# Performance work log

Measured on AMD Instinct MI355X. Metric: run time of the kernel, lower is better.

The kernel has to match this reference:

```python
import jax, jax.numpy as jnp
import numpy as np

EPS = float(np.finfo(np.float32).eps)
BN_EPS = 1e-5
TOP_K = 3


def _dist_squared(p1, p2):
    # p1: [B,N,3], p2: [B,S,3] -> [B,N,S]
    d = -2.0 * jnp.einsum('bnc,bsc->bns', p1, p2)
    d = d + jnp.sum(p1 * p1, axis=-1, keepdims=True)
    d = d + jnp.sum(p2 * p2, axis=-1)[:, None, :]
    return d


def _bn_gelu(x, gamma, beta):
    # training-mode BatchNorm1d over (batch, points), then exact GELU
    m = jnp.mean(x, axis=(0, 1))
    v = jnp.var(x, axis=(0, 1))
    xn = (x - m) * jax.lax.rsqrt(v + BN_EPS)
    return jax.nn.gelu(xn * gamma + beta, approximate=False)


def setup_inputs() -> dict:
    key = jax.random.key(0)
    ks = jax.random.split(key, 8)
    B, S, N, F, C = 8, 2048, 8192, 256, 128
    d_in, d_h, d_out = C + F, 512, 512
    return {
        'super_xyz': jax.random.normal(ks[0], (B, S, 3), jnp.float32),
        'super_point_features': jax.random.normal(ks[1], (B, S, F), jnp.float32),
        'xyz': jax.random.normal(ks[2], (B, N, 3), jnp.float32),
        'point_features': jax.random.normal(ks[3], (B, N, C), jnp.float32),
        'W1': jax.random.normal(ks[4], (d_in, d_h), jnp.float32) * 0.02,
        'g1': jnp.ones((d_h,), jnp.float32),
        'b1': jnp.zeros((d_h,), jnp.float32),
        'W2': jax.random.normal(ks[5], (d_h, d_out), jnp.float32) * 0.02,
        'g2': jnp.ones((d_out,), jnp.float32),
        'b2': jnp.zeros((d_out,), jnp.float32),
    }


def reference(super_xyz, super_point_features, xyz, point_features,
              W1, g1, b1, W2, g2, b2):
    d2 = _dist_squared(xyz, super_xyz)                 # [B,N,S]
    neg_vals, idx = jax.lax.top_k(-d2, TOP_K)          # smallest-k
    dists = jnp.maximum(-neg_vals, 0.0)                # [B,N,K]
    w = 1.0 / (dists + EPS)
    w = w / jnp.sum(w, axis=2, keepdims=True)
    gathered = jax.vmap(lambda f, i: f[i])(super_point_features, idx)  # [B,N,K,F]
    interp = jnp.sum(gathered * w[..., None], axis=2)  # [B,N,F]
    x = jnp.concatenate([point_features, interp], axis=-1)
    x = _bn_gelu(x @ W1, g1, b1)
    x = _bn_gelu(x @ W2, g2, b2)
    return x
```

## Files before the change

kernel.cpp:

```cpp
#include <hip/hip_runtime.h>
#include <hip/hip_bf16.h>


#define MROWS 65536
#define SPTS  2048
#define NPTS  8192
#define NCHUNK 8
#define CHUNK  (SPTS / NCHUNK)
#define EPSF  1.1920928955078125e-07f

typedef __bf16 v8bf __attribute__((ext_vector_type(8)));
typedef float  v4f  __attribute__((ext_vector_type(4)));

__device__ __forceinline__ float bf2f(unsigned short u) {
    union { unsigned u; float f; } v; v.u = ((unsigned)u) << 16; return v.f;
}
__device__ __forceinline__ unsigned short f2bf(float f) {
    union { float f; unsigned u; } v; v.f = f;
    unsigned r = v.u + 0x7fffu + ((v.u >> 16) & 1u);
    return (unsigned short)(r >> 16);
}
__device__ __forceinline__ float2 bf2x(unsigned u) {
    union { unsigned q; float f; } lo, hi;
    lo.q = u << 16; hi.q = u & 0xffff0000u;
    return make_float2(lo.f, hi.f);
}
__device__ __forceinline__ float ldf(const void* p, size_t i, bool bf) {
    return bf ? bf2f(((const unsigned short*)p)[i]) : ((const float*)p)[i];
}
__device__ __forceinline__ bool is_bf16_flag(const unsigned* dt) {
    return *dt == 0x3F803F80u;
}
__device__ __forceinline__ void gld16(const unsigned short* g, unsigned short* l) {
    __builtin_amdgcn_global_load_lds((const __attribute__((address_space(1))) void*)g,
                                     (__attribute__((address_space(3))) void*)l, 16, 0, 0);
}
__device__ __forceinline__ unsigned wmix(unsigned a, unsigned b, unsigned c,
                                         float w0, float w1, float w2) {
    float2 fa = bf2x(a), fb = bf2x(b), fc = bf2x(c);
    float lo = w0 * fa.x + w1 * fb.x + w2 * fc.x;
    float hi = w0 * fa.y + w1 * fb.y + w2 * fc.y;
    return ((unsigned)f2bf(hi) << 16) | (unsigned)f2bf(lo);
}
__device__ __forceinline__ uint2 pack4(float4 v) {
    uint2 r;
    r.x = ((unsigned)f2bf(v.y) << 16) | (unsigned)f2bf(v.x);
    r.y = ((unsigned)f2bf(v.w) << 16) | (unsigned)f2bf(v.z);
    return r;
}

__global__ __launch_bounds__(256) void transpose_w(const void* __restrict__ W,
                                                   unsigned short* __restrict__ WT,
                                                   int K, int N, const unsigned* dt) {
    bool bf = is_bf16_flag(dt);
    int idx = blockIdx.x * 256 + threadIdx.x;
    if (idx >= K * N) return;
    int n = idx / K, k = idx - n * K;
    WT[idx] = f2bf(ldf(W, (size_t)k * N + n, bf));
}

__global__ __launch_bounds__(256) void knn_scan(const void* __restrict__ sxyz_g,
                                                const void* __restrict__ xyz_g,
                                                double* __restrict__ pd,
                                                int* __restrict__ pi,
                                                const unsigned* dt) {
    const bool bf = is_bf16_flag(dt);
    __shared__ double sx[CHUNK], sy[CHUNK], sz[CHUNK], sn[CHUNK];
    const int b = blockIdx.y, c = blockIdx.z, tid = threadIdx.x;

    {
        int s = c * CHUNK + tid;
        size_t off = ((size_t)b * SPTS + s) * 3;
        float x, y, z;
        if (bf) {
            const unsigned short* p = (const unsigned short*)sxyz_g + off;
            x = bf2f(p[0]); y = bf2f(p[1]); z = bf2f(p[2]);
        } else {
            const float* p = (const float*)sxyz_g + off;
            x = p[0]; y = p[1]; z = p[2];
        }
        double dx = (double)x, dy = (double)y, dz = (double)z;
        sx[tid] = dx; sy[tid] = dy; sz[tid] = dz;
        sn[tid] = dx * dx + dy * dy + dz * dz;
    }
    __syncthreads();

    const int n = blockIdx.x * 256 + tid;
    size_t poff = ((size_t)b * NPTS + n) * 3;
    float px, py, pz;
    if (bf) {
        const unsigned short* p = (const unsigned short*)xyz_g + poff;
        px = bf2f(p[0]); py = bf2f(p[1]); pz = bf2f(p[2]);
    } else {
        const float* p = (const float*)xyz_g + poff;
        px = p[0]; py = p[1]; pz = p[2];
    }
    const double pxd = (double)px, pyd = (double)py, pzd = (double)pz;
    const double n1 = pxd * pxd + pyd * pyd + pzd * pzd;

    double d0 = 1e300, d1 = 1e300, d2 = 1e300;
    int i0 = 0, i1 = 0, i2 = 0;
    #pragma unroll 4
    for (int s = 0; s < CHUNK; ++s) {
        double dot = pxd * sx[s] + pyd * sy[s] + pzd * sz[s];
        double d = -2.0 * dot + n1 + sn[s];
        if (d < d2) {
            int gi = c * CHUNK + s;
            if (d < d1) {
                d2 = d1; i2 = i1;
                if (d < d0) { d1 = d0; i1 = i0; d0 = d; i0 = gi; }
                else        { d1 = d;  i1 = gi; }
            } else { d2 = d; i2 = gi; }
        }
    }
    size_t base = ((size_t)c * MROWS + (size_t)b * NPTS + n) * 3;
    pd[base] = d0; pd[base + 1] = d1; pd[base + 2] = d2;
    pi[base] = i0; pi[base + 1] = i1; pi[base + 2] = i2;
}

__global__ __launch_bounds__(256) void knn_weights(const double* __restrict__ pd,
                                                   const int* __restrict__ pi,
                                                   char* __restrict__ wi) {
    const int g = blockIdx.x * 256 + threadIdx.x;

    double d0 = 1e300, d1 = 1e300, d2 = 1e300;
    int i0 = 0, i1 = 0, i2 = 0;
    #pragma unroll
    for (int c = 0; c < NCHUNK; ++c) {
        size_t base = ((size_t)c * MROWS + g) * 3;
        #pragma unroll
        for (int j = 0; j < 3; ++j) {
            double d = pd[base + j];
            int gi = pi[base + j];
            if (d < d2) {
                if (d < d1) {
                    d2 = d1; i2 = i1;
                    if (d < d0) { d1 = d0; i1 = i0; d0 = d; i0 = gi; }
                    else        { d1 = d;  i1 = gi; }
                } else { d2 = d; i2 = gi; }
            }
        }
    }
    d0 = d0 > 0.0 ? d0 : 0.0;
    d1 = d1 > 0.0 ? d1 : 0.0;
    d2 = d2 > 0.0 ? d2 : 0.0;
    const double ED = (double)EPSF;
    double w0d = 1.0 / (d0 + ED), w1d = 1.0 / (d1 + ED), w2d = 1.0 / (d2 + ED);
    double wsd = w0d + w1d + w2d;
    float w0 = (float)(w0d / wsd), w1 = (float)(w1d / wsd), w2 = (float)(w2d / wsd);

    uint4 iv; iv.x = (unsigned)i0; iv.y = (unsigned)i1; iv.z = (unsigned)i2; iv.w = 0u;
    float4 wv = make_float4(w0, w1, w2, 0.0f);
    *(uint4*)(wi + (size_t)g * 32) = iv;
    *(float4*)(wi + (size_t)g * 32 + 16) = wv;
}

__global__ __launch_bounds__(256) void knn_interp(const char* __restrict__ wi,
                                                  const void* __restrict__ spf_g,
                                                  const void* __restrict__ pf_g,
                                                  unsigned short* __restrict__ x0,
                                                  const unsigned* dt) {
    const bool bf = is_bf16_flag(dt);
    const int tid = threadIdx.x;
    const int pl  = tid >> 4;
    const int sub = tid & 15;
    const int g   = blockIdx.x * 16 + pl;
    const int b   = g >> 13;

    const uint4  iv = *(const uint4*)(wi + (size_t)g * 32);
    const float4 wv = *(const float4*)(wi + (size_t)g * 32 + 16);
    const int i0 = (int)iv.x, i1 = (int)iv.y, i2 = (int)iv.z;
    const float w0 = wv.x, w1 = wv.y, w2 = wv.z;

    unsigned short* xr = x0 + (size_t)g * 384;
    uint4* xo = (uint4*)xr;

    if (bf) {
        const uint4* pp = (const uint4*)((const unsigned short*)pf_g + (size_t)g * 128);
        xo[sub] = pp[sub];
        const unsigned short* sb = (const unsigned short*)spf_g + (size_t)b * SPTS * 256;
        const uint4* fa = (const uint4*)(sb + (size_t)i0 * 256);
        const uint4* fb = (const uint4*)(sb + (size_t)i1 * 256);
        const uint4* fc = (const uint4*)(sb + (size_t)i2 * 256);
        #pragma unroll
        for (int r = 0; r < 2; ++r) {
            int j = sub + 16 * r;
            uint4 ua = fa[j], ub = fb[j], uc = fc[j], o;
            o.x = wmix(ua.x, ub.x, uc.x, w0, w1, w2);
            o.y = wmix(ua.y, ub.y, uc.y, w0, w1, w2);
            o.z = wmix(ua.z, ub.z, uc.z, w0, w1, w2);
            o.w = wmix(ua.w, ub.w, uc.w, w0, w1, w2);
            xo[16 + j] = o;
        }
    } else {
        const float4* pp = (const float4*)((const float*)pf_g + (size_t)g * 128);
        float4 v0 = pp[2 * sub], v1 = pp[2 * sub + 1];
        uint2 pa = pack4(v0), pb = pack4(v1);
        uint4 w; w.x = pa.x; w.y = pa.y; w.z = pb.x; w.w = pb.y;
        xo[sub] = w;
        const float* sb = (const float*)spf_g + (size_t)b * SPTS * 256;
        const float4* fa = (const float4*)(sb + (size_t)i0 * 256);
        const float4* fb = (const float4*)(sb + (size_t)i1 * 256);
        const float4* fc = (const float4*)(sb + (size_t)i2 * 256);
        #pragma unroll
        for (int r = 0; r < 2; ++r) {
            int j = sub + 16 * r;
            float4 a0 = fa[2 * j], a1 = fa[2 * j + 1];
            float4 b0 = fb[2 * j], b1 = fb[2 * j + 1];
            float4 c0 = fc[2 * j], c1 = fc[2 * j + 1];
            float4 r0, r1;
            r0.x = w0 * a0.x + w1 * b0.x + w2 * c0.x;
            r0.y = w0 * a0.y + w1 * b0.y + w2 * c0.y;
            r0.z = w0 * a0.z + w1 * b0.z + w2 * c0.z;
            r0.w = w0 * a0.w + w1 * b0.w + w2 * c0.w;
            r1.x = w0 * a1.x + w1 * b1.x + w2 * c1.x;
            r1.y = w0 * a1.y + w1 * b1.y + w2 * c1.y;
            r1.z = w0 * a1.z + w1 * b1.z + w2 * c1.z;
            r1.w = w0 * a1.w + w1 * b1.w + w2 * c1.w;
            uint2 q0 = pack4(r0), q1 = pack4(r1);
            uint4 o; o.x = q0.x; o.y = q0.y; o.z = q1.x; o.w = q1.y;
            xo[16 + j] = o;
        }
    }
}

template<bool CF32>
__global__ __launch_bounds__(256) void gemm_bt(const unsigned short* __restrict__ A,
                                               const unsigned short* __restrict__ BT,
                                               void* __restrict__ C,
                                               int M, int N, int K) {
    __shared__ unsigned short As[128 * 32];
    __shared__ unsigned short Bs[128 * 32];
    const int tid = threadIdx.x;
    const int m0 = blockIdx.x * 128, n0 = blockIdx.y * 128;
    const int lane = tid & 63, wave = tid >> 6;
    const int wm = (wave >> 1) * 64, wn = (wave & 1) * 64;
    const int l15 = lane & 15, quad = lane >> 4;

    const int o0 = tid * 16, o1 = o0 + 4096;
    const int ar0 = o0 >> 6, ac0 = (o0 & 63) >> 1;
    const int ar1 = o1 >> 6, ac1 = (o1 & 63) >> 1;
    const unsigned short* a0 = A + (size_t)(m0 + ar0) * K + ac0;
    const unsigned short* a1 = A + (size_t)(m0 + ar1) * K + ac1;
    const unsigned short* b0 = BT + (size_t)(n0 + ar0) * K + ac0;
    const unsigned short* b1 = BT + (size_t)(n0 + ar1) * K + ac1;
    unsigned short* la0 = &As[o0 >> 1];
    unsigned short* la1 = &As[o1 >> 1];
    unsigned short* lb0 = &Bs[o0 >> 1];
    unsigned short* lb1 = &Bs[o1 >> 1];

    v4f acc[4][4] = {};
    for (int k0 = 0; k0 < K; k0 += 32) {
        gld16(a0 + k0, la0);
        gld16(a1 + k0, la1);
        gld16(b0 + k0, lb0);
        gld16(b1 + k0, lb1);
        __syncthreads();
        v8bf af[4], bfr[4];
        #pragma unroll
        for (int t = 0; t < 4; ++t)
            af[t] = *(const v8bf*)&As[(wm + t * 16 + l15) * 32 + quad * 8];
        #pragma unroll
        for (int u = 0; u < 4; ++u)
            bfr[u] = *(const v8bf*)&Bs[(wn + u * 16 + l15) * 32 + quad * 8];
        #pragma unroll
        for (int t = 0; t < 4; ++t)
            #pragma unroll
            for (int u = 0; u < 4; ++u)
                acc[t][u] = __builtin_amdgcn_mfma_f32_16x16x32_bf16(af[t], bfr[u], acc[t][u], 0, 0, 0);
        __syncthreads();
    }
    #pragma unroll
    for (int t = 0; t < 4; ++t) {
        int row = m0 + wm + t * 16 + quad * 4;
        #pragma unroll
        for (int u = 0; u < 4; ++u) {
            int col = n0 + wn + u * 16 + l15;
            #pragma unroll
            for (int r = 0; r < 4; ++r) {
                if (CF32) ((float*)C)[(size_t)(row + r) * N + col] = acc[t][u][r];
                else ((unsigned short*)C)[(size_t)(row + r) * N + col] = f2bf(acc[t][u][r]);
            }
        }
    }
}

template<bool F32>
__global__ __launch_bounds__(256) void bn_stats(const void* __restrict__ yv,
                                                float* __restrict__ gsum,
                                                float* __restrict__ gsq) {
    __shared__ float ps[4][512];
    __shared__ float pq[4][512];
    const int tid = threadIdx.x;
    const int rof = tid >> 6, cb = tid & 63;
    const int r0 = blockIdx.x * 256;
    float s[8] = {0, 0, 0, 0, 0, 0, 0, 0}, q[8] = {0, 0, 0, 0, 0, 0, 0, 0};
    for (int i = 0; i < 64; ++i) {
        int row = r0 + rof + i * 4;
        float vals[8];
        if (F32) {
            const float4* yp = (const float4*)((const float*)yv + (size_t)row * 512 + cb * 8);
            float4 v0 = yp[0], v1 = yp[1];
            vals[0] = v0.x; vals[1] = v0.y; vals[2] = v0.z; vals[3] = v0.w;
            vals[4] = v1.x; vals[5] = v1.y; vals[6] = v1.z; vals[7] = v1.w;
        } else {
            uint4 v = *(const uint4*)((const unsigned short*)yv + (size_t)row * 512 + cb * 8);
            float2 f0 = bf2x(v.x), f1 = bf2x(v.y), f2 = bf2x(v.z), f3 = bf2x(v.w);
            vals[0] = f0.x; vals[1] = f0.y; vals[2] = f1.x; vals[3] = f1.y;
            vals[4] = f2.x; vals[5] = f2.y; vals[6] = f3.x; vals[7] = f3.y;
        }
        #pragma unroll
        for (int j = 0; j < 8; ++j) { s[j] += vals[j]; q[j] += vals[j] * vals[j]; }
    }
    #pragma unroll
    for (int j = 0; j < 8; ++j) { ps[rof][cb * 8 + j] = s[j]; pq[rof][cb * 8 + j] = q[j]; }
    __syncthreads();
    for (int c = tid; c < 512; c += 256) {
        float ss = ps[0][c] + ps[1][c] + ps[2][c] + ps[3][c];
        float qq = pq[0][c] + pq[1][c] + pq[2][c] + pq[3][c];
        atomicAdd(&gsum[c], ss);
        atomicAdd(&gsq[c], qq);
    }
}

__global__ __launch_bounds__(256) void bn_finalize(float* __restrict__ gsum, float* __restrict__ gsq,
                                                   float* __restrict__ scale, float* __restrict__ shift,
                                                   const void* __restrict__ g, const void* __restrict__ bta,
                                                   const unsigned* dt, float invM) {
    bool bf = is_bf16_flag(dt);
    int c = blockIdx.x * 256 + threadIdx.x;
    float mean = gsum[c] * invM;
    float var  = gsq[c] * invM - mean * mean;
    float rstd = rsqrtf(var + 1e-5f);
    float gv = ldf(g, c, bf), bv = ldf(bta, c, bf);
    scale[c] = gv * rstd;
    shift[c] = bv - mean * gv * rstd;
    gsum[c] = 0.0f; gsq[c] = 0.0f;
}

template<bool F32IN>
__global__ __launch_bounds__(256) void bn_gelu(const void* __restrict__ yv,
                                               const float* __restrict__ scale,
                                               const float* __restrict__ shift,
                                               void* __restrict__ outp,
                                               const unsigned* dt) {
    bool outf32 = false;
    if (dt) outf32 = !is_bf16_flag(dt);
    size_t gid = (size_t)blockIdx.x * 256 + threadIdx.x;
    size_t base = gid * 8;
    int c0 = (int)(base & 511);
    float in[8];
    if (F32IN) {
        const float4* yp = (const float4*)((const float*)yv + base);
        float4 v0 = yp[0], v1 = yp[1];
        in[0] = v0.x; in[1] = v0.y; in[2] = v0.z; in[3] = v0.w;
        in[4] = v1.x; in[5] = v1.y; in[6] = v1.z; in[7] = v1.w;
    } else {
        uint4 v = *(const uint4*)((const unsigned short*)yv + base);
        float2 f0 = bf2x(v.x), f1 = bf2x(v.y), f2 = bf2x(v.z), f3 = bf2x(v.w);
        in[0] = f0.x; in[1] = f0.y; in[2] = f1.x; in[3] = f1.y;
        in[4] = f2.x; in[5] = f2.y; in[6] = f3.x; in[7] = f3.y;
    }
    float4 sc0 = *(const float4*)&scale[c0];
    float4 sc1 = *(const float4*)&scale[c0 + 4];
    float4 sh0 = *(const float4*)&shift[c0];
    float4 sh1 = *(const float4*)&shift[c0 + 4];
    float sc[8] = {sc0.x, sc0.y, sc0.z, sc0.w, sc1.x, sc1.y, sc1.z, sc1.w};
    float sh[8] = {sh0.x, sh0.y, sh0.z, sh0.w, sh1.x, sh1.y, sh1.z, sh1.w};
    float o[8];
    #pragma unroll
    for (int j = 0; j < 8; ++j) {
        float x = in[j] * sc[j] + sh[j];
        o[j] = 0.5f * x * (1.0f + erff(x * 0.70710678118654752f));
    }
    if (!outf32) {
        uint4 w;
        w.x = ((unsigned)f2bf(o[1]) << 16) | (unsigned)f2bf(o[0]);
        w.y = ((unsigned)f2bf(o[3]) << 16) | (unsigned)f2bf(o[2]);
        w.z = ((unsigned)f2bf(o[5]) << 16) | (unsigned)f2bf(o[4]);
        w.w = ((unsigned)f2bf(o[7]) << 16) | (unsigned)f2bf(o[6]);
        *(uint4*)((unsigned short*)outp + base) = w;
    } else {
        float4 w0 = make_float4(o[0], o[1], o[2], o[3]);
        float4 w1 = make_float4(o[4], o[5], o[6], o[7]);
        ((float4*)outp)[gid * 2] = w0;
        ((float4*)outp)[gid * 2 + 1] = w1;
    }
}

extern "C" void kernel_launch(void* const* d_in, const int* in_sizes, int n_in,
                              void* d_out, int out_size, void* d_ws, size_t ws_size,
                              hipStream_t stream) {
    const void* sxyz = d_in[0];
    const void* spf  = d_in[1];
    const void* xyz  = d_in[2];
    const void* pf   = d_in[3];
    const void* W1   = d_in[4];
    const unsigned* dt = (const unsigned*)d_in[5];
    const void* b1   = d_in[6];
    const void* W2   = d_in[7];
    const void* g2   = d_in[8];
    const void* b2   = d_in[9];

    char* ws = (char*)d_ws;
    const size_t X0_BYTES = 50331648;
    const size_t YF_BYTES = 134217728;
    const size_t PD_BYTES = (size_t)MROWS * NCHUNK * 3 * 8;
    const size_t PI_BYTES = (size_t)MROWS * NCHUNK * 3 * 4;
    const size_t WI_BYTES = (size_t)MROWS * 32;
    const size_t NEED_F32 = X0_BYTES + YF_BYTES + 393216 + 524288 + 8192;

    if (ws_size >= NEED_F32) {
        unsigned short* x0  = (unsigned short*)ws;
        float* yF           = (float*)(ws + X0_BYTES);
        double* pd          = (double*)(ws + X0_BYTES);
        int* pi             = (int*)(ws + X0_BYTES + PD_BYTES);
        char* wi            = (char*)(ws + X0_BYTES + PD_BYTES + PI_BYTES);
        unsigned short* w1t = (unsigned short*)(ws + X0_BYTES + YF_BYTES);
        unsigned short* w2t = (unsigned short*)(ws + X0_BYTES + YF_BYTES + 393216);
        float* stats        = (float*)(ws + X0_BYTES + YF_BYTES + 393216 + 524288);
        float* gsum = stats, *gsq = stats + 512, *scale = stats + 1024, *shift = stats + 1536;
        unsigned short* x1 = (unsigned short*)d_out;

        hipMemsetAsync(gsum, 0, 4096, stream);
        transpose_w<<<dim3((384 * 512 + 255) / 256), 256, 0, stream>>>(W1, w1t, 384, 512, dt);
        transpose_w<<<dim3((512 * 512 + 255) / 256), 256, 0, stream>>>(W2, w2t, 512, 512, dt);
        knn_scan<<<dim3(32, 8, NCHUNK), 256, 0, stream>>>(sxyz, xyz, pd, pi, dt);
        knn_weights<<<dim3(256), 256, 0, stream>>>(pd, pi, wi);
        knn_interp<<<dim3(4096), 256, 0, stream>>>(wi, spf, pf, x0, dt);
        gemm_bt<true><<<dim3(512, 4), 256, 0, stream>>>(x0, w1t, yF, MROWS, 512, 384);
        bn_stats<true><<<256, 256, 0, stream>>>(yF, gsum, gsq);
        bn_finalize<<<2, 256, 0, stream>>>(gsum, gsq, scale, shift, d_in[5], b1, dt, 1.0f / 65536.0f);
        bn_gelu<true><<<16384, 256, 0, stream>>>(yF, scale, shift, x1, nullptr);
        gemm_bt<true><<<dim3(512, 4), 256, 0, stream>>>(x1, w2t, yF, MROWS, 512, 512);
        bn_stats<true><<<256, 256, 0, stream>>>(yF, gsum, gsq);
        bn_finalize<<<2, 256, 0, stream>>>(gsum, gsq, scale, shift, g2, b2, dt, 1.0f / 65536.0f);
        bn_gelu<true><<<16384, 256, 0, stream>>>(yF, scale, shift, d_out, dt);
    } else {
        unsigned short* x0  = (unsigned short*)ws;
        unsigned short* y2  = (unsigned short*)ws;
        char* wi            = (char*)(ws + X0_BYTES);
        unsigned short* w1t = (unsigned short*)(ws + 67108864);
        unsigned short* w2t = (unsigned short*)(ws + 67108864 + 393216);
        float* stats = (float*)(ws + 67108864 + 393216 + 524288);
        float* gsum = stats, *gsq = stats + 512, *scale = stats + 1024, *shift = stats + 1536;
        double* pd = (double*)(ws + 67108864 + 393216 + 524288 + 8192);
        int* pi    = (int*)(ws + 67108864 + 393216 + 524288 + 8192 + PD_BYTES);
        unsigned short* y1 = (unsigned short*)d_out;

        hipMemsetAsync(gsum, 0, 4096, stream);
        transpose_w<<<dim3((384 * 512 + 255) / 256), 256, 0, stream>>>(W1, w1t, 384, 512, dt);
        transpose_w<<<dim3((512 * 512 + 255) / 256), 256, 0, stream>>>(W2, w2t, 512, 512, dt);
        knn_scan<<<dim3(32, 8, NCHUNK), 256, 0, stream>>>(sxyz, xyz, pd, pi, dt);
        knn_weights<<<dim3(256), 256, 0, stream>>>(pd, pi, wi);
        knn_interp<<<dim3(4096), 256, 0, stream>>>(wi, spf, pf, x0, dt);
        gemm_bt<false><<<dim3(512, 4), 256, 0, stream>>>(x0, w1t, y1, MROWS, 512, 384);
        bn_stats<false><<<256, 256, 0, stream>>>(y1, gsum, gsq);
        bn_finalize<<<2, 256, 0, stream>>>(gsum, gsq, scale, shift, d_in[5], b1, dt, 1.0f / 65536.0f);
        bn_gelu<false><<<16384, 256, 0, stream>>>(y1, scale, shift, y1, nullptr);
        gemm_bt<false><<<dim3(512, 4), 256, 0, stream>>>(y1, w2t, y2, MROWS, 512, 512);
        bn_stats<false><<<256, 256, 0, stream>>>(y2, gsum, gsq);
        bn_finalize<<<2, 256, 0, stream>>>(gsum, gsq, scale, shift, g2, b2, dt, 1.0f / 65536.0f);
        bn_gelu<false><<<16384, 256, 0, stream>>>(y2, scale, shift, d_out, dt);
    }
}
```

Before: 535.4 us.

## Fuse BN statistics into GEMM epilogue and restructure kNN scan for two points

The separate bn_stats kernels are removed. Per-column sums and sums of squares are now reduced from the MFMA accumulators inside the GEMM epilogue, using shuffles and shared memory followed by global atomics, which avoids re-reading the 64K x 512 activation. The kNN scan now processes two query points per thread against a packed double4 shared array holding the pre-scaled coordinates and the norm. It uses fused multiply-adds and adds the query norm after selection, which halves the shared loads per distance. The trade-offs are more atomics and extra epilogue work in the GEMM, higher register pressure in the scan, and a small change in floating-point rounding order.

Measured after the change: 515.6 us. 1.04x faster.

```diff
diff --git a/kernel.cpp b/kernel.cpp
--- a/kernel.cpp
+++ b/kernel.cpp
@@ -65,7 +65,7 @@
                                                 int* __restrict__ pi,
                                                 const unsigned* dt) {
     const bool bf = is_bf16_flag(dt);
-    __shared__ double sx[CHUNK], sy[CHUNK], sz[CHUNK], sn[CHUNK];
+    __shared__ double4 sc[CHUNK];
     const int b = blockIdx.y, c = blockIdx.z, tid = threadIdx.x;
 
     {
@@ -80,42 +80,65 @@
             x = p[0]; y = p[1]; z = p[2];
         }
         double dx = (double)x, dy = (double)y, dz = (double)z;
-        sx[tid] = dx; sy[tid] = dy; sz[tid] = dz;
-        sn[tid] = dx * dx + dy * dy + dz * dz;
+        double4 v;
+        v.x = -2.0 * dx; v.y = -2.0 * dy; v.z = -2.0 * dz;
+        v.w = dx * dx + dy * dy + dz * dz;
+        sc[tid] = v;
     }
     __syncthreads();
 
-    const int n = blockIdx.x * 256 + tid;
-    size_t poff = ((size_t)b * NPTS + n) * 3;
-    float px, py, pz;
-    if (bf) {
-        const unsigned short* p = (const unsigned short*)xyz_g + poff;
-        px = bf2f(p[0]); py = bf2f(p[1]); pz = bf2f(p[2]);
-    } else {
-        const float* p = (const float*)xyz_g + poff;
-        px = p[0]; py = p[1]; pz = p[2];
-    }
-    const double pxd = (double)px, pyd = (double)py, pzd = (double)pz;
-    const double n1 = pxd * pxd + pyd * pyd + pzd * pzd;
-
-    double d0 = 1e300, d1 = 1e300, d2 = 1e300;
-    int i0 = 0, i1 = 0, i2 = 0;
+    const int nA = blockIdx.x * 512 + tid;
+    const int nB = nA + 256;
+    double ax, ay, az, bx, by, bz;
+    {
+        size_t offA = ((size_t)b * NPTS + nA) * 3;
+        size_t offB = ((size_t)b * NPTS + nB) * 3;
+        if (bf) {
+            const unsigned short* pA = (const unsigned short*)xyz_g + offA;
+            const unsigned short* pB = (const unsigned short*)xyz_g + offB;
+            ax = (double)bf2f(pA[0]); ay = (double)bf2f(pA[1]); az = (double)bf2f(pA[2]);
+            bx = (double)bf2f(pB[0]); by = (double)bf2f(pB[1]); bz = (double)bf2f(pB[2]);
+        } else {
+            const float* pA = (const float*)xyz_g + offA;
+            const float* pB = (const float*)xyz_g + offB;
+            ax = (double)pA[0]; ay = (double)pA[1]; az = (double)pA[2];
+            bx = (double)pB[0]; by = (double)pB[1]; bz = (double)pB[2];
+        }
+    }
+    const double na = ax * ax + ay * ay + az * az;
+    const double nb = bx * bx + by * by + bz * bz;
+
+    double a0 = 1e300, a1 = 1e300, a2 = 1e300;
+    double q0 = 1e300, q1 = 1e300, q2 = 1e300;
+    int ai0 = 0, ai1 = 0, ai2 = 0, bi0 = 0, bi1 = 0, bi2 = 0;
     #pragma unroll 4
     for (int s = 0; s < CHUNK; ++s) {
-        double dot = pxd * sx[s] + pyd * sy[s] + pzd * sz[s];
-        double d = -2.0 * dot + n1 + sn[s];
-        if (d < d2) {
+        double4 v = sc[s];
+        double da = fma(ax, v.x, fma(ay, v.y, fma(az, v.z, v.w)));
+        double db = fma(bx, v.x, fma(by, v.y, fma(bz, v.z, v.w)));
+        if (da < a2) {
             int gi = c * CHUNK + s;
-            if (d < d1) {
-                d2 = d1; i2 = i1;
-                if (d < d0) { d1 = d0; i1 = i0; d0 = d; i0 = gi; }
-                else        { d1 = d;  i1 = gi; }
-            } else { d2 = d; i2 = gi; }
-        }
-    }
-    size_t base = ((size_t)c * MROWS + (size_t)b * NPTS + n) * 3;
-    pd[base] = d0; pd[base + 1] = d1; pd[base + 2] = d2;
-    pi[base] = i0; pi[base + 1] = i1; pi[base + 2] = i2;
+            if (da < a1) {
+                a2 = a1; ai2 = ai1;
+                if (da < a0) { a1 = a0; ai1 = ai0; a0 = da; ai0 = gi; }
+                else         { a1 = da; ai1 = gi; }
+            } else { a2 = da; ai2 = gi; }
+        }
+        if (db < q2) {
+            int gi = c * CHUNK + s;
+            if (db < q1) {
+                q2 = q1; bi2 = bi1;
+                if (db < q0) { q1 = q0; bi1 = bi0; q0 = db; bi0 = gi; }
+                else         { q1 = db; bi1 = gi; }
+            } else { q2 = db; bi2 = gi; }
+        }
+    }
+    size_t baseA = ((size_t)c * MROWS + (size_t)b * NPTS + nA) * 3;
+    size_t baseB = ((size_t)c * MROWS + (size_t)b * NPTS + nB) * 3;
+    pd[baseA] = a0 + na; pd[baseA + 1] = a1 + na; pd[baseA + 2] = a2 + na;
+    pi[baseA] = ai0; pi[baseA + 1] = ai1; pi[baseA + 2] = ai2;
+    pd[baseB] = q0 + nb; pd[baseB + 1] = q1 + nb; pd[baseB + 2] = q2 + nb;
+    pi[baseB] = bi0; pi[baseB + 1] = bi1; pi[baseB + 2] = bi2;
 }
 
 __global__ __launch_bounds__(256) void knn_weights(const double* __restrict__ pd,
@@ -217,8 +240,8 @@
             r1.y = w0 * a1.y + w1 * b1.y + w2 * c1.y;
             r1.z = w0 * a1.z + w1 * b1.z + w2 * c1.z;
             r1.w = w0 * a1.w + w1 * b1.w + w2 * c1.w;
-            uint2 q0 = pack4(r0), q1 = pack4(r1);
-            uint4 o; o.x = q0.x; o.y = q0.y; o.z = q1.x; o.w = q1.y;
+            uint2 p0 = pack4(r0), p1 = pack4(r1);
+            uint4 o; o.x = p0.x; o.y = p0.y; o.z = p1.x; o.w = p1.y;
             xo[16 + j] = o;
         }
     }
@@ -228,7 +251,9 @@
 __global__ __launch_bounds__(256) void gemm_bt(const unsigned short* __restrict__ A,
                                                const unsigned short* __restrict__ BT,
                                                void* __restrict__ C,
-                                               int M, int N, int K) {
+                                               int M, int N, int K,
+                                               float* __restrict__ gsum,
+                                               float* __restrict__ gsq) {
     __shared__ unsigned short As[128 * 32];
     __shared__ unsigned short Bs[128 * 32];
     const int tid = threadIdx.x;
@@ -283,43 +308,44 @@
             }
         }
     }
-}
-
-template<bool F32>
-__global__ __launch_bounds__(256) void bn_stats(const void* __restrict__ yv,
-                                                float* __restrict__ gsum,
-                                                float* __restrict__ gsq) {
-    __shared__ float ps[4][512];
-    __shared__ float pq[4][512];
-    const int tid = threadIdx.x;
-    const int rof = tid >> 6, cb = tid & 63;
-    const int r0 = blockIdx.x * 256;
-    float s[8] = {0, 0, 0, 0, 0, 0, 0, 0}, q[8] = {0, 0, 0, 0, 0, 0, 0, 0};
-    for (int i = 0; i < 64; ++i) {
-        int row = r0 + rof + i * 4;
-        float vals[8];
-        if (F32) {
-            const float4* yp = (const float4*)((const float*)yv + (size_t)row * 512 + cb * 8);
-            float4 v0 = yp[0], v1 = yp[1];
-            vals[0] = v0.x; vals[1] = v0.y; vals[2] = v0.z; vals[3] = v0.w;
-            vals[4] = v1.x; vals[5] = v1.y; vals[6] = v1.z; vals[7] = v1.w;
-        } else {
-            uint4 v = *(const uint4*)((const unsigned short*)yv + (size_t)row * 512 + cb * 8);
-            float2 f0 = bf2x(v.x), f1 = bf2x(v.y), f2 = bf2x(v.z), f3 = bf2x(v.w);
-            vals[0] = f0.x; vals[1] = f0.y; vals[2] = f1.x; vals[3] = f1.y;
-            vals[4] = f2.x; vals[5] = f2.y; vals[6] = f3.x; vals[7] = f3.y;
-        }
-        #pragma unroll
-        for (int j = 0; j < 8; ++j) { s[j] += vals[j]; q[j] += vals[j] * vals[j]; }
-    }
+
+    float s4[4], q4[4];
     #pragma unroll
-    for (int j = 0; j < 8; ++j) { ps[rof][cb * 8 + j] = s[j]; pq[rof][cb * 8 + j] = q[j]; }
+    for (int u = 0; u < 4; ++u) {
+        float s = 0.0f, q = 0.0f;
+        #pragma unroll
+        for (int t = 0; t < 4; ++t)
+            #pragma unroll
+            for (int r = 0; r < 4; ++r) {
+                float v = acc[t][u][r];
+                s += v; q += v * v;
+            }
+        s4[u] = s; q4[u] = q;
+    }
+    #pragma unroll
+    for (int u = 0; u < 4; ++u) {
+        s4[u] += __shfl_xor(s4[u], 16);
+        s4[u] += __shfl_xor(s4[u], 32);
+        q4[u] += __shfl_xor(q4[u], 16);
+        q4[u] += __shfl_xor(q4[u], 32);
+    }
+    float* cs = (float*)As;
+    float* cq = (float*)Bs;
     __syncthreads();
-    for (int c = tid; c < 512; c += 256) {
-        float ss = ps[0][c] + ps[1][c] + ps[2][c] + ps[3][c];
-        float qq = pq[0][c] + pq[1][c] + pq[2][c] + pq[3][c];
-        atomicAdd(&gsum[c], ss);
-        atomicAdd(&gsq[c], qq);
+    if (quad == 0) {
+        #pragma unroll
+        for (int u = 0; u < 4; ++u) {
+            cs[wave * 64 + u * 16 + l15] = s4[u];
+            cq[wave * 64 + u * 16 + l15] = q4[u];
+        }
+    }
+    __syncthreads();
+    if (tid < 128) {
+        int hf = tid >> 6, idx = tid & 63;
+        float ss = cs[hf * 64 + idx] + cs[(hf + 2) * 64 + idx];
+        float qq = cq[hf * 64 + idx] + cq[(hf + 2) * 64 + idx];
+        atomicAdd(&gsum[n0 + tid], ss);
+        atomicAdd(&gsq[n0 + tid], qq);
     }
 }
 
@@ -407,7 +433,6 @@
     const size_t YF_BYTES = 134217728;
     const size_t PD_BYTES = (size_t)MROWS * NCHUNK * 3 * 8;
     const size_t PI_BYTES = (size_t)MROWS * NCHUNK * 3 * 4;
-    const size_t WI_BYTES = (size_t)MROWS * 32;
     const size_t NEED_F32 = X0_BYTES + YF_BYTES + 393216 + 524288 + 8192;
 
     if (ws_size >= NEED_F32) {
@@ -425,15 +450,13 @@
         hipMemsetAsync(gsum, 0, 4096, stream);
         transpose_w<<<dim3((384 * 512 + 255) / 256), 256, 0, stream>>>(W1, w1t, 384, 512, dt);
         transpose_w<<<dim3((512 * 512 + 255) / 256), 256, 0, stream>>>(W2, w2t, 512, 512, dt);
-        knn_scan<<<dim3(32, 8, NCHUNK), 256, 0, stream>>>(sxyz, xyz, pd, pi, dt);
+        knn_scan<<<dim3(16, 8, NCHUNK), 256, 0, stream>>>(sxyz, xyz, pd, pi, dt);
         knn_weights<<<dim3(256), 256, 0, stream>>>(pd, pi, wi);
         knn_interp<<<dim3(4096), 256, 0, stream>>>(wi, spf, pf, x0, dt);
-        gemm_bt<true><<<dim3(512, 4), 256, 0, stream>>>(x0, w1t, yF, MROWS, 512, 384);
-        bn_stats<true><<<256, 256, 0, stream>>>(yF, gsum, gsq);
+        gemm_bt<true><<<dim3(512, 4), 256, 0, stream>>>(x0, w1t, yF, MROWS, 512, 384, gsum, gsq);
         bn_finalize<<<2, 256, 0, stream>>>(gsum, gsq, scale, shift, d_in[5], b1, dt, 1.0f / 65536.0f);
         bn_gelu<true><<<16384, 256, 0, stream>>>(yF, scale, shift, x1, nullptr);
-        gemm_bt<true><<<dim3(512, 4), 256, 0, stream>>>(x1, w2t, yF, MROWS, 512, 512);
-        bn_stats<true><<<256, 256, 0, stream>>>(yF, gsum, gsq);
+        gemm_bt<true><<<dim3(512, 4), 256, 0, stream>>>(x1, w2t, yF, MROWS, 512, 512, gsum, gsq);
         bn_finalize<<<2, 256, 0, stream>>>(gsum, gsq, scale, shift, g2, b2, dt, 1.0f / 65536.0f);
         bn_gelu<true><<<16384, 256, 0, stream>>>(yF, scale, shift, d_out, dt);
     } else {
@@ -451,15 +474,13 @@
         hipMemsetAsync(gsum, 0, 4096, stream);
         transpose_w<<<dim3((384 * 512 + 255) / 256), 256, 0, stream>>>(W1, w1t, 384, 512, dt);
         transpose_w<<<dim3((512 * 512 + 255) / 256), 256, 0, stream>>>(W2, w2t, 512, 512, dt);
-        knn_scan<<<dim3(32, 8, NCHUNK), 256, 0, stream>>>(sxyz, xyz, pd, pi, dt);
+        knn_scan<<<dim3(16, 8, NCHUNK), 256, 0, stream>>>(sxyz, xyz, pd, pi, dt);
         knn_weights<<<dim3(256), 256, 0, stream>>>(pd, pi, wi);
         knn_interp<<<dim3(4096), 256, 0, stream>>>(wi, spf, pf, x0, dt);
-        gemm_bt<false><<<dim3(512, 4), 256, 0, stream>>>(x0, w1t, y1, MROWS, 512, 384);
-        bn_stats<false><<<256, 256, 0, stream>>>(y1, gsum, gsq);
+        gemm_bt<false><<<dim3(512, 4), 256, 0, stream>>>(x0, w1t, y1, MROWS, 512, 384, gsum, gsq);
         bn_finalize<<<2, 256, 0, stream>>>(gsum, gsq, scale, shift, d_in[5], b1, dt, 1.0f / 65536.0f);
         bn_gelu<false><<<16384, 256, 0, stream>>>(y1, scale, shift, y1, nullptr);
-        gemm_bt<false><<<dim3(512, 4), 256, 0, stream>>>(y1, w2t, y2, MROWS, 512, 512);
-        bn_stats<false><<<256, 256, 0, stream>>>(y2, gsum, gsq);
+        gemm_bt<false><<<dim3(512, 4), 256, 0, stream>>>(y1, w2t, y2, MROWS, 512, 512, gsum, gsq);
         bn_finalize<<<2, 256, 0, stream>>>(gsum, gsq, scale, shift, g2, b2, dt, 1.0f / 65536.0f);
         bn_gelu<false><<<16384, 256, 0, stream>>>(y2, scale, shift, d_out, dt);
     }
```
